# Kernel tuning notes

Hardware: AMD Instinct MI355X
Metric: run time of the kernel (lower is better)

Reference implementation:

```python
import jax, jax.numpy as jnp
import numpy as np

B, C, H, W = 4, 256, 64, 64


def setup_inputs() -> dict:
    key = jax.random.key(0)
    ks = jax.random.split(key, 8)
    s = 0.02
    return {
        "x": jax.random.normal(ks[0], (B, C, H, W), dtype=jnp.float32),
        "Wq": jax.random.normal(ks[1], (C, C), dtype=jnp.float32) * s,
        "bq": jax.random.normal(ks[2], (C,), dtype=jnp.float32) * s,
        "Wk": jax.random.normal(ks[3], (C, C), dtype=jnp.float32) * s,
        "bk": jax.random.normal(ks[4], (C,), dtype=jnp.float32) * s,
        "Wv": jax.random.normal(ks[5], (C, C), dtype=jnp.float32) * s,
        "bv": jax.random.normal(ks[6], (C,), dtype=jnp.float32) * s,
        "gamma": jax.random.normal(ks[7], (1,), dtype=jnp.float32),
    }


def reference(x, Wq, bq, Wk, bk, Wv, bv, gamma):
    b, c, h, w = x.shape
    n = h * w
    xf = x.reshape(b, c, n)  # [B,C,N]
    # 1x1 convs == per-pixel linear over channels
    q = jnp.einsum("oc,bcn->bon", Wq, xf) + bq[None, :, None]  # [B,C,N]
    k = jnp.einsum("oc,bcn->bon", Wk, xf) + bk[None, :, None]  # [B,C,N]
    v = jnp.einsum("oc,bcn->bon", Wv, xf) + bv[None, :, None]  # [B,C,N]
    # energy[b,i,j] = sum_c q[b,c,i] * k[b,c,j]  (Q^T K, no scale in original)
    energy = jnp.einsum("bci,bcj->bij", q, k)  # [B,N,N]
    attention = jax.nn.softmax(energy, axis=-1)  # softmax over j
    # out = V @ attention^T : out[b,c,i] = sum_j v[b,c,j] * attention[b,i,j]
    out = jnp.einsum("bcj,bij->bci", v, attention)  # [B,C,N]
    out = gamma[0] * out + xf
    return out.reshape(b, c, h, w)
```

## Files before the change

### kernel.cpp

```cpp
#include <hip/hip_runtime.h>
#include <hip/hip_bf16.h>

#define Bb 4
#define Cc 256
#define Nn 4096
#define NV 4160

typedef short s16x8 __attribute__((ext_vector_type(8)));
typedef float f32x4 __attribute__((ext_vector_type(4)));

__device__ __forceinline__ unsigned short f2bf(float f) {
    unsigned u = __builtin_bit_cast(unsigned, f);
    u += 0x7FFFu + ((u >> 16) & 1u);
    return (unsigned short)(u >> 16);
}

__device__ __forceinline__ f32x4 mfma16(s16x8 a, s16x8 b, f32x4 c) {
    return __builtin_amdgcn_mfma_f32_16x16x32_bf16(a, b, c, 0, 0, 0);
}

#if __has_builtin(__builtin_amdgcn_global_load_lds)
#define GL16(g, sdst)                                                              \
    __builtin_amdgcn_global_load_lds(                                              \
        (const __attribute__((address_space(1))) unsigned int*)(g),                \
        (__attribute__((address_space(3))) unsigned int*)(sdst), 16, 0, 0)
#else
#define GL16(g, sdst)                                                              \
    do {                                                                           \
        *(s16x8*)((char*)(sdst) + (threadIdx.x & 63) * 16) = *(const s16x8*)(g);   \
    } while (0)
#endif

__global__ void prep_w(const float* __restrict__ Wq, const float* __restrict__ Wk,
                       const float* __restrict__ Wv, unsigned short* __restrict__ Wbf) {
    int idx = (blockIdx.x * 256 + threadIdx.x) * 8;
    int mat = idx >> 16;
    int off = idx & 65535;
    const float* src = (mat == 0) ? Wq : ((mat == 1) ? Wk : Wv);
    float4 a = *(const float4*)(src + off);
    float4 b = *(const float4*)(src + off + 4);
    s16x8 o;
    o[0] = (short)f2bf(a.x); o[1] = (short)f2bf(a.y);
    o[2] = (short)f2bf(a.z); o[3] = (short)f2bf(a.w);
    o[4] = (short)f2bf(b.x); o[5] = (short)f2bf(b.y);
    o[6] = (short)f2bf(b.z); o[7] = (short)f2bf(b.w);
    *(s16x8*)(Wbf + idx) = o;
}

__global__ void transpose_x(const float* __restrict__ x, unsigned short* __restrict__ xT) {
    int b = blockIdx.z, c0 = blockIdx.y * 64, n0 = blockIdx.x * 64;
    __shared__ float tile[64][65];
    int t = threadIdx.x;
    int r = t >> 2, q = t & 3;
    const float* src = x + ((size_t)(b * Cc + c0 + r)) * Nn + n0 + q * 16;
#pragma unroll
    for (int j = 0; j < 4; j++) {
        float4 v4 = *(const float4*)(src + j * 4);
        tile[r][q * 16 + j * 4 + 0] = v4.x;
        tile[r][q * 16 + j * 4 + 1] = v4.y;
        tile[r][q * 16 + j * 4 + 2] = v4.z;
        tile[r][q * 16 + j * 4 + 3] = v4.w;
    }
    __syncthreads();
    unsigned short* dst = xT + ((size_t)b * Nn + n0 + r) * Cc + c0 + q * 16;
    s16x8 o0, o1;
#pragma unroll
    for (int j = 0; j < 8; j++) o0[j] = (short)f2bf(tile[q * 16 + j][r]);
#pragma unroll
    for (int j = 0; j < 8; j++) o1[j] = (short)f2bf(tile[q * 16 + 8 + j][r]);
    *(s16x8*)dst = o0;
    *(s16x8*)(dst + 8) = o1;
}

__global__ void proj(const unsigned short* __restrict__ xT, const unsigned short* __restrict__ Wbf,
                     const float* __restrict__ bq, const float* __restrict__ bk,
                     const float* __restrict__ bv,
                     unsigned short* __restrict__ qT, unsigned short* __restrict__ kT,
                     unsigned short* __restrict__ vO) {
    int nt0 = blockIdx.x * 64;
    int mat = blockIdx.y;
    int b   = blockIdx.z;
    int t = threadIdx.x, w = t >> 6, l = t & 63;
    int lr = l & 15, lg = l >> 4;
    const unsigned short* Wm  = Wbf + mat * (Cc * Cc);
    const float* bias = (mat == 0) ? bq : ((mat == 1) ? bk : bv);
    const unsigned short* xTb = xT + (size_t)b * Nn * Cc;

    if (mat < 2) {
        unsigned short* out = ((mat == 0) ? qT : kT) + (size_t)b * Nn * Cc;
        int nrow = nt0 + w * 16;
        s16x8 af[8];
#pragma unroll
        for (int kk = 0; kk < 8; kk++)
            af[kk] = *(const s16x8*)(xTb + (nrow + lr) * Cc + kk * 32 + lg * 8);
        for (int ct = 0; ct < 16; ct++) {
            f32x4 acca = {0, 0, 0, 0}, accb = {0, 0, 0, 0};
#pragma unroll
            for (int kk = 0; kk < 8; kk += 2) {
                s16x8 bfa = *(const s16x8*)(Wm + (ct * 16 + lr) * Cc + kk * 32 + lg * 8);
                s16x8 bfb = *(const s16x8*)(Wm + (ct * 16 + lr) * Cc + (kk + 1) * 32 + lg * 8);
                acca = mfma16(af[kk], bfa, acca);
                accb = mfma16(af[kk + 1], bfb, accb);
            }
            f32x4 acc = acca + accb;
            float bb = bias[ct * 16 + lr];
#pragma unroll
            for (int r = 0; r < 4; r++)
                out[(nrow + lg * 4 + r) * Cc + ct * 16 + lr] = f2bf(acc[r] + bb);
        }
    } else {
        unsigned short* out = vO + (size_t)b * Cc * NV;
        for (int mt = 0; mt < 4; mt++) {
            int crow = (w * 4 + mt) * 16;
            s16x8 af[8];
#pragma unroll
            for (int kk = 0; kk < 8; kk++)
                af[kk] = *(const s16x8*)(Wm + (crow + lr) * Cc + kk * 32 + lg * 8);
#pragma unroll
            for (int nt = 0; nt < 4; nt++) {
                f32x4 acca = {0, 0, 0, 0}, accb = {0, 0, 0, 0};
#pragma unroll
                for (int kk = 0; kk < 8; kk += 2) {
                    s16x8 bfa = *(const s16x8*)(xTb + (nt0 + nt * 16 + lr) * Cc + kk * 32 + lg * 8);
                    s16x8 bfb = *(const s16x8*)(xTb + (nt0 + nt * 16 + lr) * Cc + (kk + 1) * 32 + lg * 8);
                    acca = mfma16(af[kk], bfa, acca);
                    accb = mfma16(af[kk + 1], bfb, accb);
                }
                f32x4 acc = acca + accb;
#pragma unroll
                for (int r = 0; r < 4; r++) {
                    float bb = bias[crow + lg * 4 + r];
                    out[(size_t)(crow + lg * 4 + r) * NV + nt0 + nt * 16 + lr] = f2bf(acc[r] + bb);
                }
            }
        }
    }
}

__global__ void __launch_bounds__(256, 1)
attn(const unsigned short* __restrict__ qT, const unsigned short* __restrict__ kT,
     const unsigned short* __restrict__ vv,
     float* __restrict__ OPT, float* __restrict__ lp) {
    int id = blockIdx.x;
    int bs = id & 7, b = bs >> 1, s = bs & 1, iblk = id >> 3;
    int t = threadIdx.x, w = t >> 6, l = t & 63;
    int lr = l & 15, lg = l >> 4;
    int i0 = iblk * 128 + w * 32;

    __shared__ char Ks[2][16384];
    __shared__ char Vs[2][16384];
    __shared__ unsigned short P_lds[4][2][512];
    unsigned short* plA = P_lds[w][0];
    unsigned short* plB = P_lds[w][1];

    const unsigned short* qb = qT + ((size_t)b * Nn + i0) * Cc;
    const char* kbase = (const char*)(kT + ((size_t)b * Nn + s * 2048) * Cc);
    const char* vbase = (const char*)(vv + (size_t)b * Cc * NV + s * 2048);

    s16x8 qfA[8], qfB[8];
#pragma unroll
    for (int kk = 0; kk < 8; kk++) {
        qfA[kk] = *(const s16x8*)(qb + lr * Cc + kk * 32 + lg * 8);
        qfB[kk] = *(const s16x8*)(qb + (16 + lr) * Cc + kk * 32 + lg * 8);
    }

    f32x4 OA[16], OB[16];
#pragma unroll
    for (int ct = 0; ct < 16; ct++) { OA[ct] = {0, 0, 0, 0}; OB[ct] = {0, 0, 0, 0}; }
    float lsA[4] = {0, 0, 0, 0}, lsB[4] = {0, 0, 0, 0};
    const float L2E = 1.44269504088896340736f;

#define STAGEK(bufi, jt)                                                        \
    {                                                                           \
        const char* ksl_ = kbase + (size_t)(jt) * 16384;                        \
        _Pragma("unroll") for (int i_ = 0; i_ < 4; i_++) {                      \
            int chunk_ = w * 4 + i_;                                            \
            int L_ = chunk_ * 1024 + l * 16;                                    \
            int row_ = L_ >> 9;                                                 \
            GL16(ksl_ + (L_ ^ ((row_ & 7) << 4)), &Ks[bufi][chunk_ * 1024]);    \
        }                                                                       \
    }

#define STAGEV(bufi, jt)                                                        \
    {                                                                           \
        _Pragma("unroll") for (int i_ = 0; i_ < 4; i_++) {                      \
            int chunk_ = w * 4 + i_;                                            \
            int row_ = chunk_ * 16 + (l >> 2);                                  \
            int colb_ = ((l & 3) * 16) ^ (((l >> 3) & 3) << 4);                 \
            GL16(vbase + (size_t)row_ * (NV * 2) + (size_t)(jt) * 64 + colb_,   \
                 &Vs[bufi][chunk_ * 1024]);                                     \
        }                                                                       \
    }

    STAGEK(0, 0);
    STAGEV(0, 0);
    asm volatile("s_waitcnt vmcnt(0)" ::: "memory");
    __syncthreads();
    int buf = 0;

    for (int jt = 0; jt < 64; jt++) {
        if (jt < 63) {
            STAGEK(buf ^ 1, jt + 1);
            STAGEV(buf ^ 1, jt + 1);
        }
        const char* ksb = Ks[buf];
        f32x4 EA0 = {0, 0, 0, 0}, EA1 = {0, 0, 0, 0};
        f32x4 EB0 = {0, 0, 0, 0}, EB1 = {0, 0, 0, 0};
#pragma unroll
        for (int kk = 0; kk < 8; kk++) {
            int cb = (kk * 64 + lg * 16) ^ ((lr & 7) << 4);
            s16x8 k0 = *(const s16x8*)(ksb + lr * 512 + cb);
            s16x8 k1 = *(const s16x8*)(ksb + (16 + lr) * 512 + cb);
            EA0 = mfma16(qfA[kk], k0, EA0);
            EA1 = mfma16(qfA[kk], k1, EA1);
            EB0 = mfma16(qfB[kk], k0, EB0);
            EB1 = mfma16(qfB[kk], k1, EB1);
        }
        float pA0[4], pA1[4], pB0[4], pB1[4];
#pragma unroll
        for (int r = 0; r < 4; r++) {
            pA0[r] = exp2f(EA0[r] * L2E);
            pA1[r] = exp2f(EA1[r] * L2E);
            pB0[r] = exp2f(EB0[r] * L2E);
            pB1[r] = exp2f(EB1[r] * L2E);
            lsA[r] += pA0[r] + pA1[r];
            lsB[r] += pB0[r] + pB1[r];
        }
#pragma unroll
        for (int r = 0; r < 4; r++) {
            plA[(lg * 4 + r) * 32 + lr] = f2bf(pA0[r]);
            plA[(lg * 4 + r) * 32 + 16 + lr] = f2bf(pA1[r]);
            plB[(lg * 4 + r) * 32 + lr] = f2bf(pB0[r]);
            plB[(lg * 4 + r) * 32 + 16 + lr] = f2bf(pB1[r]);
        }
        asm volatile("s_waitcnt lgkmcnt(0)" ::: "memory");
        __builtin_amdgcn_sched_barrier(0);
        s16x8 pfA = *(const s16x8*)(plA + lr * 32 + lg * 8);
        s16x8 pfB = *(const s16x8*)(plB + lr * 32 + lg * 8);
        const char* vsb = Vs[buf];
        int vswz = (lg * 16) ^ (((lr >> 1) & 3) << 4);
#pragma unroll
        for (int ct = 0; ct < 16; ct++) {
            s16x8 vf = *(const s16x8*)(vsb + (ct * 16 + lr) * 64 + vswz);
            OA[ct] = mfma16(pfA, vf, OA[ct]);
            OB[ct] = mfma16(pfB, vf, OB[ct]);
        }
        asm volatile("s_waitcnt vmcnt(0)" ::: "memory");
        __syncthreads();
        buf ^= 1;
    }

#pragma unroll
    for (int r = 0; r < 4; r++) {
#pragma unroll
        for (int msk = 1; msk <= 8; msk <<= 1) {
            lsA[r] += __shfl_xor(lsA[r], msk);
            lsB[r] += __shfl_xor(lsB[r], msk);
        }
    }
    size_t sb = (size_t)(s * Bb + b);
    if (lr == 0) {
#pragma unroll
        for (int r = 0; r < 4; r++) {
            lp[sb * Nn + i0 + lg * 4 + r] = lsA[r];
            lp[sb * Nn + i0 + 16 + lg * 4 + r] = lsB[r];
        }
    }
    float* ob = OPT + sb * Nn * Cc;
#pragma unroll
    for (int ct = 0; ct < 16; ct++) {
#pragma unroll
        for (int r = 0; r < 4; r++) {
            ob[(size_t)(i0 + lg * 4 + r) * Cc + ct * 16 + lr] = OA[ct][r];
            ob[(size_t)(i0 + 16 + lg * 4 + r) * Cc + ct * 16 + lr] = OB[ct][r];
        }
    }
#undef STAGEK
#undef STAGEV
}

__global__ void __launch_bounds__(256)
merge(const float* __restrict__ OPT, const float* __restrict__ lp,
      const float* __restrict__ x, const float* __restrict__ gamma,
      float* __restrict__ out) {
    int b = blockIdx.z, c0 = blockIdx.y * 64, n0 = blockIdx.x * 64;
    __shared__ float tile[64][65];
    __shared__ float linv[64];
    int t = threadIdx.x;
    if (t < 64) {
        float sum = lp[(size_t)b * Nn + n0 + t] + lp[(size_t)(Bb + b) * Nn + n0 + t];
        linv[t] = 1.0f / sum;
    }
    __syncthreads();
    float g = gamma[0];
    int r = t >> 2, q = t & 3;
    const float* p0 = OPT + ((size_t)b * Nn + n0 + r) * Cc + c0 + q * 16;
    const float* p1 = OPT + ((size_t)(Bb + b) * Nn + n0 + r) * Cc + c0 + q * 16;
    float sc = g * linv[r];
#pragma unroll
    for (int j = 0; j < 4; j++) {
        float4 a0 = *(const float4*)(p0 + j * 4);
        float4 a1 = *(const float4*)(p1 + j * 4);
        tile[r][q * 16 + j * 4 + 0] = sc * (a0.x + a1.x);
        tile[r][q * 16 + j * 4 + 1] = sc * (a0.y + a1.y);
        tile[r][q * 16 + j * 4 + 2] = sc * (a0.z + a1.z);
        tile[r][q * 16 + j * 4 + 3] = sc * (a0.w + a1.w);
    }
    __syncthreads();
    const float* xp = x + ((size_t)b * Cc + c0 + r) * Nn + n0 + q * 16;
    float* op = out + ((size_t)b * Cc + c0 + r) * Nn + n0 + q * 16;
#pragma unroll
    for (int j = 0; j < 4; j++) {
        float4 xv = *(const float4*)(xp + j * 4);
        float4 o4;
        o4.x = tile[q * 16 + j * 4 + 0][r] + xv.x;
        o4.y = tile[q * 16 + j * 4 + 1][r] + xv.y;
        o4.z = tile[q * 16 + j * 4 + 2][r] + xv.z;
        o4.w = tile[q * 16 + j * 4 + 3][r] + xv.w;
        *(float4*)(op + j * 4) = o4;
    }
}

extern "C" void kernel_launch(void* const* d_in, const int* in_sizes, int n_in,
                              void* d_out, int out_size, void* d_ws, size_t ws_size,
                              hipStream_t stream) {
    (void)in_sizes; (void)n_in; (void)out_size; (void)ws_size;
    const float* x     = (const float*)d_in[0];
    const float* Wq    = (const float*)d_in[1];
    const float* bq    = (const float*)d_in[2];
    const float* Wk    = (const float*)d_in[3];
    const float* bk    = (const float*)d_in[4];
    const float* Wv    = (const float*)d_in[5];
    const float* bv    = (const float*)d_in[6];
    const float* gamma = (const float*)d_in[7];
    float* out = (float*)d_out;

    const size_t XTN = (size_t)Bb * Nn * Cc;
    const size_t VSZ = (size_t)Bb * Cc * NV;
    unsigned short* xT  = (unsigned short*)d_ws;
    unsigned short* Wbf = xT + XTN;
    unsigned short* qT  = Wbf + 3 * Cc * Cc;
    unsigned short* kT  = qT + XTN;
    unsigned short* vv  = kT + XTN;
    float*          OPT = (float*)(vv + VSZ);
    float*          lp  = OPT + 2 * XTN;

    hipLaunchKernelGGL(prep_w, dim3(96), dim3(256), 0, stream, Wq, Wk, Wv, Wbf);
    hipLaunchKernelGGL(transpose_x, dim3(Nn / 64, Cc / 64, Bb), dim3(256), 0, stream, x, xT);
    hipLaunchKernelGGL(proj, dim3(Nn / 64, 3, Bb), dim3(256), 0, stream,
                       xT, Wbf, bq, bk, bv, qT, kT, vv);
    hipLaunchKernelGGL(attn, dim3(256), dim3(256), 0, stream,
                       qT, kT, vv, OPT, lp);
    hipLaunchKernelGGL(merge, dim3(Nn / 64, Cc / 64, Bb), dim3(256), 0, stream,
                       OPT, lp, x, gamma, out);
}
```

Before: 202.3 us.

## Split attention keys four ways, double grid, and prefetch V fragments

The attention kernel now splits the key dimension into four partitions instead of two, so it launches 512 blocks with occupancy hint 2, and maps block ids so each XCD handles one batch. The merge kernel sums four partial outputs and row sums instead of two. V fragments are loaded into registers before the LDS wait so their latency overlaps the P writes. Workspace is re-laid out with OPT aliasing xT and the V padding removed, which raises partial-output traffic and register pressure and risks LDS bank conflicts on V.

```diff
diff --git a/kernel.cpp b/kernel.cpp
--- a/kernel.cpp
+++ b/kernel.cpp
@@ -4,7 +4,7 @@
 #define Bb 4
 #define Cc 256
 #define Nn 4096
-#define NV 4160
+#define NV 4096
 
 typedef short s16x8 __attribute__((ext_vector_type(8)));
 typedef float f32x4 __attribute__((ext_vector_type(4)));
@@ -137,12 +137,15 @@
     }
 }
 
-__global__ void __launch_bounds__(256, 1)
+__global__ void __launch_bounds__(256, 2)
 attn(const unsigned short* __restrict__ qT, const unsigned short* __restrict__ kT,
      const unsigned short* __restrict__ vv,
      float* __restrict__ OPT, float* __restrict__ lp) {
     int id = blockIdx.x;
-    int bs = id & 7, b = bs >> 1, s = bs & 1, iblk = id >> 3;
+    int xcd = id & 7, k = id >> 3;
+    int combo = xcd * 2 + (k & 1);
+    int b = combo >> 2, s = combo & 3;
+    int iblk = k >> 1;
     int t = threadIdx.x, w = t >> 6, l = t & 63;
     int lr = l & 15, lg = l >> 4;
     int i0 = iblk * 128 + w * 32;
@@ -154,8 +157,8 @@
     unsigned short* plB = P_lds[w][1];
 
     const unsigned short* qb = qT + ((size_t)b * Nn + i0) * Cc;
-    const char* kbase = (const char*)(kT + ((size_t)b * Nn + s * 2048) * Cc);
-    const char* vbase = (const char*)(vv + (size_t)b * Cc * NV + s * 2048);
+    const char* kbase = (const char*)(kT + ((size_t)b * Nn + s * 1024) * Cc);
+    const char* vbase = (const char*)(vv + (size_t)b * Cc * NV + s * 1024);
 
     s16x8 qfA[8], qfB[8];
 #pragma unroll
@@ -198,8 +201,8 @@
     __syncthreads();
     int buf = 0;
 
-    for (int jt = 0; jt < 64; jt++) {
-        if (jt < 63) {
+    for (int jt = 0; jt < 32; jt++) {
+        if (jt < 31) {
             STAGEK(buf ^ 1, jt + 1);
             STAGEV(buf ^ 1, jt + 1);
         }
@@ -233,17 +236,20 @@
             plB[(lg * 4 + r) * 32 + lr] = f2bf(pB0[r]);
             plB[(lg * 4 + r) * 32 + 16 + lr] = f2bf(pB1[r]);
         }
+        const char* vsb = Vs[buf];
+        int vswz = (lg * 16) ^ (((lr >> 1) & 3) << 4);
+        s16x8 vfr[16];
+#pragma unroll
+        for (int ct = 0; ct < 16; ct++)
+            vfr[ct] = *(const s16x8*)(vsb + (ct * 16 + lr) * 64 + vswz);
         asm volatile("s_waitcnt lgkmcnt(0)" ::: "memory");
         __builtin_amdgcn_sched_barrier(0);
         s16x8 pfA = *(const s16x8*)(plA + lr * 32 + lg * 8);
         s16x8 pfB = *(const s16x8*)(plB + lr * 32 + lg * 8);
-        const char* vsb = Vs[buf];
-        int vswz = (lg * 16) ^ (((lr >> 1) & 3) << 4);
 #pragma unroll
         for (int ct = 0; ct < 16; ct++) {
-            s16x8 vf = *(const s16x8*)(vsb + (ct * 16 + lr) * 64 + vswz);
-            OA[ct] = mfma16(pfA, vf, OA[ct]);
-            OB[ct] = mfma16(pfB, vf, OB[ct]);
+            OA[ct] = mfma16(pfA, vfr[ct], OA[ct]);
+            OB[ct] = mfma16(pfB, vfr[ct], OB[ct]);
         }
         asm volatile("s_waitcnt vmcnt(0)" ::: "memory");
         __syncthreads();
@@ -288,23 +294,30 @@
     __shared__ float linv[64];
     int t = threadIdx.x;
     if (t < 64) {
-        float sum = lp[(size_t)b * Nn + n0 + t] + lp[(size_t)(Bb + b) * Nn + n0 + t];
+        float sum = 0.f;
+#pragma unroll
+        for (int si = 0; si < 4; si++)
+            sum += lp[(size_t)(si * Bb + b) * Nn + n0 + t];
         linv[t] = 1.0f / sum;
     }
     __syncthreads();
     float g = gamma[0];
     int r = t >> 2, q = t & 3;
-    const float* p0 = OPT + ((size_t)b * Nn + n0 + r) * Cc + c0 + q * 16;
-    const float* p1 = OPT + ((size_t)(Bb + b) * Nn + n0 + r) * Cc + c0 + q * 16;
     float sc = g * linv[r];
 #pragma unroll
     for (int j = 0; j < 4; j++) {
-        float4 a0 = *(const float4*)(p0 + j * 4);
-        float4 a1 = *(const float4*)(p1 + j * 4);
-        tile[r][q * 16 + j * 4 + 0] = sc * (a0.x + a1.x);
-        tile[r][q * 16 + j * 4 + 1] = sc * (a0.y + a1.y);
-        tile[r][q * 16 + j * 4 + 2] = sc * (a0.z + a1.z);
-        tile[r][q * 16 + j * 4 + 3] = sc * (a0.w + a1.w);
+        float4 a = {0, 0, 0, 0};
+#pragma unroll
+        for (int si = 0; si < 4; si++) {
+            const float* p = OPT + (size_t)(si * Bb + b) * Nn * Cc +
+                             ((size_t)(n0 + r)) * Cc + c0 + q * 16 + j * 4;
+            float4 v4 = *(const float4*)p;
+            a.x += v4.x; a.y += v4.y; a.z += v4.z; a.w += v4.w;
+        }
+        tile[r][q * 16 + j * 4 + 0] = sc * a.x;
+        tile[r][q * 16 + j * 4 + 1] = sc * a.y;
+        tile[r][q * 16 + j * 4 + 2] = sc * a.z;
+        tile[r][q * 16 + j * 4 + 3] = sc * a.w;
     }
     __syncthreads();
     const float* xp = x + ((size_t)b * Cc + c0 + r) * Nn + n0 + q * 16;
@@ -336,20 +349,19 @@
     float* out = (float*)d_out;
 
     const size_t XTN = (size_t)Bb * Nn * Cc;
-    const size_t VSZ = (size_t)Bb * Cc * NV;
-    unsigned short* xT  = (unsigned short*)d_ws;
-    unsigned short* Wbf = xT + XTN;
-    unsigned short* qT  = Wbf + 3 * Cc * Cc;
+    unsigned short* qT  = (unsigned short*)d_ws;
     unsigned short* kT  = qT + XTN;
     unsigned short* vv  = kT + XTN;
-    float*          OPT = (float*)(vv + VSZ);
-    float*          lp  = OPT + 2 * XTN;
+    unsigned short* xT  = vv + XTN;
+    unsigned short* Wbf = xT + XTN;
+    float*          OPT = (float*)xT;
+    float*          lp  = OPT + (size_t)16 * Nn * Cc;
 
     hipLaunchKernelGGL(prep_w, dim3(96), dim3(256), 0, stream, Wq, Wk, Wv, Wbf);
     hipLaunchKernelGGL(transpose_x, dim3(Nn / 64, Cc / 64, Bb), dim3(256), 0, stream, x, xT);
     hipLaunchKernelGGL(proj, dim3(Nn / 64, 3, Bb), dim3(256), 0, stream,
                        xT, Wbf, bq, bk, bv, qT, kT, vv);
-    hipLaunchKernelGGL(attn, dim3(256), dim3(256), 0, stream,
+    hipLaunchKernelGGL(attn, dim3(512), dim3(256), 0, stream,
                        qT, kT, vv, OPT, lp);
     hipLaunchKernelGGL(merge, dim3(Nn / 64, Cc / 64, Bb), dim3(256), 0, stream,
                        OPT, lp, x, gamma, out);
```

After: 260.8 us. 29.0% more time.
